# Optimization experiments

Hardware: AMD Instinct MI355X
Metric: run time of the kernel (lower is better)

## Reference

```python
import jax, jax.numpy as jnp
import numpy as np

N = 50000   # nodes
E = 800000  # edges (avg degree 16)
C = 64      # in_channels == out_channels


def _linear_params(key, fan_in, fan_out):
    kw, kb = jax.random.split(key)
    s = 1.0 / np.sqrt(fan_in)
    W = jax.random.uniform(kw, (fan_out, fan_in), minval=-s, maxval=s, dtype=jnp.float32)
    b = jax.random.uniform(kb, (fan_out,), minval=-s, maxval=s, dtype=jnp.float32)
    return W, b


def setup_inputs() -> dict:
    key = jax.random.key(0)
    ks = jax.random.split(key, 12)
    scalar = jax.random.normal(ks[0], (N, C), dtype=jnp.float32)
    vector = jax.random.normal(ks[1], (N, 3, C), dtype=jnp.float32)
    position = jax.random.normal(ks[2], (N, 3), dtype=jnp.float32)
    edge_index = jax.random.randint(ks[3], (2, E), 0, N, dtype=jnp.int64)
    edge_attr = jax.random.uniform(ks[4], (E,), dtype=jnp.float32)
    # Scalar_Conv params
    Wss, bss = _linear_params(ks[5], 2 * C, C)   # s_to_s
    Wvs, bvs = _linear_params(ks[6], 2 * C, C)   # v_to_s
    Wsl, bsl = _linear_params(ks[7], 2 * C, C)   # scalar_linear
    # Vector_Conv params
    Wsv, bsv = _linear_params(ks[8], 2 * C, C)   # s_to_v
    Wvv, bvv = _linear_params(ks[9], 2 * C, C)   # v_to_v
    Wvl, bvl = _linear_params(ks[10], 2 * C, C)  # vector_linear
    return dict(scalar=scalar, vector=vector, position=position,
                edge_index=edge_index, edge_attr=edge_attr,
                Wss=Wss, bss=bss, Wvs=Wvs, bvs=bvs, Wsl=Wsl, bsl=bsl,
                Wsv=Wsv, bsv=bsv, Wvv=Wvv, bvv=bvv, Wvl=Wvl, bvl=bvl)


def _norm(edge_index, edge_attr, num_nodes):
    # B=True path: edge_attr-weighted symmetric degree normalization
    row, col = edge_index[0], edge_index[1]
    deg = jax.ops.segment_sum(edge_attr, col, num_segments=num_nodes)
    deg_safe = jnp.where(deg > 0, deg, 1.0)
    dis = jnp.where(deg > 0, deg_safe ** -0.5, 0.0)
    return row, col, dis[row] * dis[col] * edge_attr


def _forward(scalar, vector, position, edge_index, edge_attr,
             Wss, bss, Wvs, bvs, Wsl, bsl, Wsv, bsv, Wvv, bvv, Wvl, bvl):
    num_nodes = scalar.shape[0]
    row, col = _norm(edge_index, edge_attr, num_nodes)[:2]
    _, _, norm = _norm(edge_index, edge_attr, num_nodes)
    # PyG: _i = target (col), _j = source (row); aggregate at col
    s_i, s_j = scalar[col], scalar[row]            # [E,C]
    v_i, v_j = vector[col], vector[row]            # [E,3,C]
    pos = position[col] - position[row]            # [E,3]
    s_cat = jnp.concatenate([s_i, s_j], axis=-1)   # [E,2C]
    v_cat = jnp.concatenate([v_i, v_j], axis=-1)   # [E,3,2C]

    # ---- Scalar_Conv messages ----
    s2s = jax.nn.silu(s_cat @ Wss.T + bss)                          # [E,C]
    v2s = v_cat @ Wvs.T + bvs                                       # [E,3,C]
    v2s = jax.nn.silu(jnp.sum(v2s * pos[:, :, None], axis=1))       # [E,C]
    s_msg = (jnp.concatenate([s2s, v2s], axis=-1) @ Wsl.T + bsl)    # [E,C]
    s_msg = norm[:, None] * s_msg
    s_agg = jax.ops.segment_sum(s_msg, col, num_segments=num_nodes)

    # ---- Vector_Conv messages ----
    s2v = s_cat @ Wsv.T + bsv                                       # [E,C]
    s2v = jnp.tanh(s2v[:, None, :] * pos[:, :, None])               # [E,3,C]
    v2v = v_cat @ Wvv.T + bvv                                       # [E,3,C]
    v_msg = jnp.concatenate([v2v, s2v], axis=-1) @ Wvl.T + bvl      # [E,3,C]
    v_msg = norm[:, None, None] * v_msg
    v_agg = jax.ops.segment_sum(v_msg, col, num_segments=num_nodes)

    scalar_out = jax.nn.silu(s_agg) + scalar
    vector_out = jnp.tanh(v_agg) + vector
    return scalar_out, vector_out


def reference(scalar, vector, position, edge_index, edge_attr,
              Wss, bss, Wvs, bvs, Wsl, bsl, Wsv, bsv, Wvv, bvv, Wvl, bvl):
    return _forward(scalar, vector, position, edge_index, edge_attr,
                    Wss, bss, Wvs, bvs, Wsl, bsl, Wsv, bsv, Wvv, bvv, Wvl, bvl)
```

## Files before the change

### kernel.cpp

```cpp
#include <hip/hip_runtime.h>
#include <cstdint>
#include <cstddef>

typedef unsigned int   u32;
typedef unsigned short u16;
typedef __attribute__((ext_vector_type(8))) short bf16x8;
typedef __attribute__((ext_vector_type(4))) float f32x4;

__device__ __forceinline__ float bf2f(u32 bits16) { return __uint_as_float(bits16 << 16); }
__device__ __forceinline__ u16 f2bf(float f) {
  u32 u = __float_as_uint(f);
  u = u + 0x7FFFu + ((u >> 16) & 1u);
  return (u16)(u >> 16);
}
__device__ __forceinline__ u32 pk(float a, float b) {
  return (u32)f2bf(a) | ((u32)f2bf(b) << 16);
}
__device__ __forceinline__ float lo16(u32 w) { return bf2f(w & 0xFFFFu); }
__device__ __forceinline__ float hi16(u32 w) { return bf2f(w >> 16); }
__device__ __forceinline__ float frcp(float x) { return __builtin_amdgcn_rcpf(x); }
__device__ __forceinline__ float fexp2(float x) { return __builtin_amdgcn_exp2f(x); }

#define NL2E   (-1.4426950408889634f)
#define TWOL2E (2.8853900817779268f)
#define CNTSC  1073741824.0

__device__ __forceinline__ int load_idx(const int* eidx, int is64, long long pos) {
  if (is64) return (int)(((const long long*)eidx)[pos]);
  return eidx[pos];
}

__global__ void k_prep1(const float* Wvl, const float* Wvv,
                        const float* bvv, const float* bvl,
                        const int* eidx, int E, int* flag,
                        float* WcTmp, float* bc,
                        double* dpk, int* erecI, int N) {
  int b = blockIdx.x, tid = threadIdx.x;
  if (b < 32) {
    int c = 2 * b + (tid >> 7), kk = tid & 127;
    float s = 0.f;
    for (int m = 0; m < 64; ++m) s += Wvl[c * 128 + m] * Wvv[m * 128 + kk];
    WcTmp[c * 128 + kk] = s;
  } else if (b == 32) {
    __shared__ int zc;
    if (tid == 0) zc = 0;
    __syncthreads();
    int n = (E < 1024) ? E : 1024;
    int local = 0;
    for (int i = tid; i < n; i += 256) {
      if (eidx[2 * i + 1] == 0) local++;
    }
    atomicAdd(&zc, local);
    __syncthreads();
    if (tid == 0) *flag = (zc >= (n >> 1)) ? 1 : 0;
  } else if (b == 33) {
    if (tid < 64) {
      float s = 0.f;
      for (int m = 0; m < 64; ++m) s += Wvl[tid * 128 + m] * bvv[m];
      bc[tid] = s + bvl[tid];
    }
  } else if (b == 34) {
    if (tid < 64) erecI[E + tid] = 0;
  } else {
    int idx = (b - 35) * 256 + tid;
    if (idx < N) dpk[idx] = 0.0;
  }
}

__global__ void k_prep2(const float* Wss, const float* Wsv, const float* Wvs,
                        const float* Wsl, const float* Wvl, const float* WcTmp,
                        u32* Wsl2, u32* Wpk, u16* Wtg) {
  int b = blockIdx.x, tid = threadIdx.x;
  if (b < 2) {
    for (int i = 0; i < 8; ++i) {
      int o = b * 2048 + i * 256 + tid;
      int h = o & 1, c = (o >> 1) & 63, g = o >> 7;
      int k = 4 * g + 2 * h;
      Wsl2[o] = pk(Wsl[c * 128 + k], Wsl[c * 128 + k + 1]);
    }
  } else if (b == 2) {
    for (int i = 0; i < 8; ++i) {
      int o = i * 256 + tid;
      int h = o & 1, c = (o >> 1) & 63, g = o >> 7;
      int k = 4 * g + 2 * h;
      Wpk[o] = pk(Wvl[c * 128 + 64 + k], Wvl[c * 128 + 64 + k + 1]);
    }
  } else {
    for (int i = 0; i < 16; ++i) {
      int p = (b - 3) * 4096 + i * 256 + tid;
      int r = p >> 6, k = p & 63;
      int g = (r >> 6) & 3, ch = r & 63;
      int src = ch * 128 + ((g & 2) ? 64 : 0) + k;
      float w;
      if (r < 256) w = (g & 1) ? Wsv[src] : Wss[src];
      else         w = (g & 1) ? WcTmp[src] : Wvs[src];
      u16 h = f2bf(w);
      Wtg[r * 128 + k] = h;
      Wtg[r * 128 + 64 + k] = f2bf(w - bf2f(h));
    }
  }
}

__global__ void k_scan_red(const double* dpk, int* blocksum, float* dis, int N) {
  __shared__ int lds[256];
  int tid = threadIdx.x, idx = blockIdx.x * 256 + tid;
  int c = 0;
  if (idx < N) {
    double p = dpk[idx];
    c = (int)(p * (1.0 / CNTSC));
    float dg = (float)(p - (double)c * CNTSC);
    dis[idx] = (dg > 0.f) ? rsqrtf(dg) : 0.f;
  }
  lds[tid] = c;
  __syncthreads();
  for (int off = 128; off > 0; off >>= 1) {
    if (tid < off) lds[tid] += lds[tid + off];
    __syncthreads();
  }
  if (tid == 0) blocksum[blockIdx.x] = lds[0];
}

__global__ void k_scan_mid(const int* blocksum, int* blockoff, int NB, int* rowptr, int N, int E) {
  __shared__ int lds[1024];
  int tid = threadIdx.x;
  int v = (tid < NB) ? blocksum[tid] : 0;
  lds[tid] = v;
  __syncthreads();
  for (int off = 1; off < 1024; off <<= 1) {
    int t = (tid >= off) ? lds[tid - off] : 0;
    __syncthreads();
    lds[tid] += t;
    __syncthreads();
  }
  if (tid < NB) blockoff[tid] = lds[tid] - v;
  if (tid == 0) rowptr[N] = E;
}

__global__ void k_scan_out(const double* dpk, const int* blockoff, int* rowptr, int* cursor, int N) {
  __shared__ int lds[256];
  int tid = threadIdx.x, idx = blockIdx.x * 256 + tid;
  int v = (idx < N) ? (int)(dpk[idx] * (1.0 / CNTSC)) : 0;
  lds[tid] = v;
  __syncthreads();
  for (int off = 1; off < 256; off <<= 1) {
    int t = (tid >= off) ? lds[tid - off] : 0;
    __syncthreads();
    lds[tid] += t;
    __syncthreads();
  }
  if (idx < N) {
    int o = blockoff[blockIdx.x] + lds[tid] - v;
    rowptr[idx] = o;
    cursor[idx] = o;
  }
}

__global__ void k_fill(const int* eidx, const int* flag, const float* attr, const float* dis,
                       const float* pos, int* cursor, float4* erecA, int* erecI, int E) {
  int e = blockIdx.x * 256 + threadIdx.x;
  if (e >= E) return;
  int is64 = *flag;
  int r  = load_idx(eidx, is64, e);
  int cl = load_idx(eidx, is64, (long long)E + e);
  float wr = dis[r] * attr[e];
  float dx = pos[cl * 3 + 0] - pos[r * 3 + 0];
  float dy = pos[cl * 3 + 1] - pos[r * 3 + 1];
  float dz = pos[cl * 3 + 2] - pos[r * 3 + 2];
  int p = atomicAdd(&cursor[cl], 1);
  erecA[p] = make_float4(wr, dx, dy, dz);
  erecI[p] = r;
}

__global__ __launch_bounds__(512, 4) void k_gemm_deg(
    const float* __restrict__ scalar, const float* __restrict__ vector,
    const u16* __restrict__ Wtg,
    uint4* __restrict__ rec_i4, uint4* __restrict__ rec_j4, int N, int GB,
    const int* __restrict__ eidx, const int* __restrict__ flag,
    const float* __restrict__ attr, double* __restrict__ dpk, int E) {
  __shared__ u32 smem[8192];
  int tid = threadIdx.x;
  if ((int)blockIdx.x >= GB) {
    int e = ((int)blockIdx.x - GB) * 512 + tid;
    if (e < E) {
      int is64 = *flag;
      int col = load_idx(eidx, is64, (long long)E + e);
      atomicAdd(&dpk[col], (double)attr[e] + CNTSC);
    }
    return;
  }
  u16*   Ax = (u16*)smem;
  float* Ep = (float*)smem;
  int lane = tid & 63, wv = tid >> 6;
  int nb = blockIdx.x * 32;

  {
    int srow = tid >> 2, skq = tid & 3;
    const float* sp;
    int snode;
    if (srow < 32) { snode = nb + srow; sp = scalar + (size_t)snode * 64 + skq * 16; }
    else {
      int d = (srow - 32) >> 5, nl2 = (srow - 32) & 31;
      snode = nb + nl2;
      sp = vector + (size_t)snode * 192 + d * 64 + skq * 16;
    }
    bool valid = snode < N;
    u16 hi[16], lo[16];
    #pragma unroll
    for (int q = 0; q < 4; ++q) {
      float4 v = valid ? *(const float4*)(sp + 4 * q) : make_float4(0.f, 0.f, 0.f, 0.f);
      float xs[4] = {v.x, v.y, v.z, v.w};
      #pragma unroll
      for (int j = 0; j < 4; ++j) {
        u16 h = f2bf(xs[j]);
        hi[4 * q + j] = h;
        lo[4 * q + j] = f2bf(xs[j] - bf2f(h));
      }
    }
    int rs = srow & 7;
    #pragma unroll
    for (int c = 0; c < 2; ++c) {
      int lc = 2 * skq + c;
      uint4 wh, wl;
      wh.x = (u32)hi[8*c+0] | ((u32)hi[8*c+1] << 16);
      wh.y = (u32)hi[8*c+2] | ((u32)hi[8*c+3] << 16);
      wh.z = (u32)hi[8*c+4] | ((u32)hi[8*c+5] << 16);
      wh.w = (u32)hi[8*c+6] | ((u32)hi[8*c+7] << 16);
      wl.x = (u32)lo[8*c+0] | ((u32)lo[8*c+1] << 16);
      wl.y = (u32)lo[8*c+2] | ((u32)lo[8*c+3] << 16);
      wl.z = (u32)lo[8*c+4] | ((u32)lo[8*c+5] << 16);
      wl.w = (u32)lo[8*c+6] | ((u32)lo[8*c+7] << 16);
      *(uint4*)(Ax + srow * 128 + (lc ^ rs) * 8)        = wh;
      *(uint4*)(Ax + srow * 128 + ((8 + lc) ^ rs) * 8)  = wl;
    }
  }
  __syncthreads();

  int c0 = wv * 32;
  int bl = lane & 15, bh = lane >> 4;
  f32x4 acc[8][2];
  #pragma unroll
  for (int mt = 0; mt < 8; ++mt)
    #pragma unroll
    for (int nt = 0; nt < 2; ++nt)
      acc[mt][nt] = (f32x4){0.f, 0.f, 0.f, 0.f};

  #pragma unroll
  for (int kh = 0; kh < 2; ++kh) {
    int k0 = kh * 32;
    bf16x8 Bh[2][2], Bl[2][2];
    #pragma unroll
    for (int rg = 0; rg < 2; ++rg)
      #pragma unroll
      for (int nt = 0; nt < 2; ++nt) {
        size_t rr = (size_t)(rg * 256 + c0 + nt * 16 + bl) * 128 + k0 + bh * 8;
        Bh[rg][nt] = *(const bf16x8*)(Wtg + rr);
        Bl[rg][nt] = *(const bf16x8*)(Wtg + rr + 64);
      }
    #pragma unroll
    for (int mt = 0; mt < 8; ++mt) {
      int row = mt * 16 + bl;
      int ch = (k0 >> 3) + bh, rs = row & 7;
      bf16x8 Ah = *(const bf16x8*)(Ax + row * 128 + (ch ^ rs) * 8);
      bf16x8 Al = *(const bf16x8*)(Ax + row * 128 + ((8 + ch) ^ rs) * 8);
      int rg = (mt < 2) ? 0 : 1;
      #pragma unroll
      for (int nt = 0; nt < 2; ++nt) {
        f32x4 a = acc[mt][nt];
        a = __builtin_amdgcn_mfma_f32_16x16x32_bf16(Ah, Bh[rg][nt], a, 0, 0, 0);
        a = __builtin_amdgcn_mfma_f32_16x16x32_bf16(Al, Bh[rg][nt], a, 0, 0, 0);
        a = __builtin_amdgcn_mfma_f32_16x16x32_bf16(Ah, Bl[rg][nt], a, 0, 0, 0);
        acc[mt][nt] = a;
      }
    }
  }

  int ech = tid & 63, eng = tid >> 6;
  uint4 oi[4], oj[4];
  #pragma unroll
  for (int pg = 0; pg < 4; ++pg) {
    __syncthreads();
    #pragma unroll
    for (int mm = 0; mm < 2; ++mm) {
      int mt = 2 * pg + mm;
      #pragma unroll
      for (int nt = 0; nt < 2; ++nt)
        #pragma unroll
        for (int r = 0; r < 4; ++r) {
          int rl = mm * 16 + bh * 4 + r;
          Ep[rl * 256 + c0 + nt * 16 + bl] = acc[mt][nt][r];
        }
    }
    __syncthreads();
    #pragma unroll
    for (int q = 0; q < 4; ++q) {
      int nl2 = eng + 8 * q;
      float vi0 = Ep[nl2 * 256 + ech];
      float vi1 = Ep[nl2 * 256 + 64 + ech];
      float vj0 = Ep[nl2 * 256 + 128 + ech];
      float vj1 = Ep[nl2 * 256 + 192 + ech];
      if (pg == 0) {
        oi[q].x = pk(vi0, vi1);                  oj[q].x = pk(vj0, vj1);
      } else if (pg == 1) {
        oi[q].y = (u32)f2bf(vi0);                oj[q].y = (u32)f2bf(vj0);
        oi[q].z = (u32)f2bf(vi1) << 16;          oj[q].z = (u32)f2bf(vj1) << 16;
      } else if (pg == 2) {
        oi[q].y |= (u32)f2bf(vi0) << 16;         oj[q].y |= (u32)f2bf(vj0) << 16;
        oi[q].w = (u32)f2bf(vi1);                oj[q].w = (u32)f2bf(vj1);
      } else {
        oi[q].z |= (u32)f2bf(vi0);               oj[q].z |= (u32)f2bf(vj0);
        oi[q].w |= (u32)f2bf(vi1) << 16;         oj[q].w |= (u32)f2bf(vj1) << 16;
      }
    }
  }
  #pragma unroll
  for (int q = 0; q < 4; ++q) {
    int node = nb + eng + 8 * q;
    if (node < N) {
      rec_i4[(size_t)node * 64 + ech] = oi[q];
      rec_j4[(size_t)node * 64 + ech] = oj[q];
    }
  }
}

__global__ __launch_bounds__(512) void k_edges(
    const u16* __restrict__ rec_i, const u16* __restrict__ rec_j,
    const float4* __restrict__ erecA, const int* __restrict__ erecI,
    const int* __restrict__ rowptr, const float* __restrict__ dis,
    const float* __restrict__ scalar, const float* __restrict__ vector,
    const float* __restrict__ bss, const float* __restrict__ bvs,
    const float* __restrict__ bsv, const float* __restrict__ bsl,
    const u32* __restrict__ Wsl2g, const u32* __restrict__ Wpkg,
    const float* __restrict__ bcg,
    float* __restrict__ out_s, float* __restrict__ out_v, int N) {
  __shared__ u32 sWsl[4096];
  __shared__ u32 sWv[2048];
  __shared__ float sStage[8 * 128];
  int tid = threadIdx.x, lane = tid & 63, wv = tid >> 6;
  for (int o = tid; o < 4096; o += 512) sWsl[o] = Wsl2g[o];
  for (int o = tid; o < 2048; o += 512) sWv[o] = Wpkg[o];
  __syncthreads();

  int node = __builtin_amdgcn_readfirstlane((int)(blockIdx.x * 8) + wv);
  if (node >= N) node = N - 1;

  uint4 riv = *(const uint4*)(rec_i + ((size_t)node << 9) + lane * 8);
  float aiB  = lo16(riv.x) + bss[lane];
  float KciB = TWOL2E * (hi16(riv.x) + bsv[lane]);
  float Bvs  = bvs[lane];
  float bib0 = lo16(riv.y) + Bvs;
  float bib1 = hi16(riv.y) + Bvs;
  float bib2 = lo16(riv.z) + Bvs;
  float Pi0  = hi16(riv.z), Pi1 = lo16(riv.w), Pi2 = hi16(riv.w);
  float bsl_c = bsl[lane], bc_c = bcg[lane];
  float disc = dis[node];

  float us = 0, uv = 0, t0 = 0, t1 = 0, t2 = 0, g0 = 0, g1 = 0, g2 = 0, wa = 0;
  int rp = rowptr[node], re = rowptr[node + 1];
  u32 lane16 = (u32)lane << 4;
  const char* rjb = (const char*)rec_j;

  u32 ra = (u32)erecI[rp];
  u32 rb = (u32)erecI[rp + 1];
  uint4 pre0 = *(const uint4*)(rjb + ((ra << 10) + lane16));
  uint4 pre1 = *(const uint4*)(rjb + ((rb << 10) + lane16));
  int p = rp;
  #define EDGE_MATH(CUR, EV)                                                  \
    {                                                                         \
      float nrm = EV.x, dx = EV.y, dy = EV.z, dz = EV.w;                      \
      float aj  = lo16(CUR.x), cj  = hi16(CUR.x);                             \
      float bj0 = lo16(CUR.y), bj1 = hi16(CUR.y), bj2 = lo16(CUR.z);          \
      float rj0 = hi16(CUR.z), rj1 = lo16(CUR.w), rj2 = hi16(CUR.w);          \
      float xs  = aiB + aj;                                                   \
      float s2s = xs * frcp(1.f + fexp2(xs * NL2E));                          \
      float yv  = (bib0 + bj0) * dx;                                          \
      yv = fmaf(bib1 + bj1, dy, yv);                                          \
      yv = fmaf(bib2 + bj2, dz, yv);                                          \
      float v2s = yv * frcp(1.f + fexp2(yv * NL2E));                          \
      float qh  = fmaf(TWOL2E, cj, KciB);                                     \
      float th0 = fmaf(-2.f, frcp(1.f + fexp2(qh * dx)), 1.f);                \
      float th1 = fmaf(-2.f, frcp(1.f + fexp2(qh * dy)), 1.f);                \
      float th2 = fmaf(-2.f, frcp(1.f + fexp2(qh * dz)), 1.f);                \
      us = fmaf(nrm, s2s, us); uv = fmaf(nrm, v2s, uv);                       \
      t0 = fmaf(nrm, th0, t0); t1 = fmaf(nrm, th1, t1); t2 = fmaf(nrm, th2, t2);\
      g0 = fmaf(nrm, rj0, g0); g1 = fmaf(nrm, rj1, g1); g2 = fmaf(nrm, rj2, g2);\
      wa += nrm;                                                              \
    }
  for (; p + 1 < re; p += 2) {
    uint4 cur0 = pre0, cur1 = pre1;
    u32 rn0 = (u32)erecI[p + 2];
    u32 rn1 = (u32)erecI[p + 3];
    pre0 = *(const uint4*)(rjb + ((rn0 << 10) + lane16));
    pre1 = *(const uint4*)(rjb + ((rn1 << 10) + lane16));
    float4 e0 = erecA[p];
    float4 e1 = erecA[p + 1];
    EDGE_MATH(cur0, e0)
    EDGE_MATH(cur1, e1)
  }
  if (p < re) {
    uint4 cur0 = pre0;
    float4 e0 = erecA[p];
    EDGE_MATH(cur0, e0)
  }
  #undef EDGE_MATH

  us *= disc; uv *= disc;
  t0 *= disc; t1 *= disc; t2 *= disc;
  g0 *= disc; g1 *= disc; g2 *= disc;
  wa *= disc;

  float* mys = &sStage[wv * 128];
  mys[lane] = us; mys[64 + lane] = uv;
  __threadfence_block();
  float acc = wa * bsl_c;
  #pragma unroll
  for (int g = 0; g < 32; ++g) {
    float4 u = *(const float4*)&mys[4 * g];
    uint2 w = *(const uint2*)&sWsl[(g * 64 + lane) * 2];
    acc = fmaf(u.x, lo16(w.x), acc);
    acc = fmaf(u.y, hi16(w.x), acc);
    acc = fmaf(u.z, lo16(w.y), acc);
    acc = fmaf(u.w, hi16(w.y), acc);
  }
  size_t so = ((size_t)node << 6) + lane;
  out_s[so] = acc * frcp(1.f + fexp2(acc * NL2E)) + scalar[so];

  float gg[3] = {g0, g1, g2}, tt[3] = {t0, t1, t2}, Pi[3] = {Pi0, Pi1, Pi2};
  #pragma unroll
  for (int d = 0; d < 3; ++d) {
    size_t vo = (((size_t)node * 3 + d) << 6) + lane;
    float vid = vector[vo];
    __threadfence_block();
    mys[lane] = tt[d];
    __threadfence_block();
    float a2 = fmaf(wa, bc_c + Pi[d], gg[d]);
    #pragma unroll
    for (int g = 0; g < 16; ++g) {
      float4 tu = *(const float4*)&mys[4 * g];
      uint2 w = *(const uint2*)&sWv[(g * 64 + lane) * 2];
      a2 = fmaf(tu.x, lo16(w.x), a2); a2 = fmaf(tu.y, hi16(w.x), a2);
      a2 = fmaf(tu.z, lo16(w.y), a2); a2 = fmaf(tu.w, hi16(w.y), a2);
    }
    float th = fmaf(-2.f, frcp(1.f + fexp2(TWOL2E * a2)), 1.f);
    out_v[vo] = th + vid;
  }
}

extern "C" void kernel_launch(void* const* d_in, const int* in_sizes, int n_in,
                              void* d_out, int out_size, void* d_ws, size_t ws_size,
                              hipStream_t stream) {
  const float* scalar   = (const float*)d_in[0];
  const float* vector   = (const float*)d_in[1];
  const float* position = (const float*)d_in[2];
  const int*   eidx     = (const int*)d_in[3];
  const float* attr     = (const float*)d_in[4];
  const float* Wss = (const float*)d_in[5];
  const float* bss = (const float*)d_in[6];
  const float* Wvs = (const float*)d_in[7];
  const float* bvs = (const float*)d_in[8];
  const float* Wsl = (const float*)d_in[9];
  const float* bsl = (const float*)d_in[10];
  const float* Wsv = (const float*)d_in[11];
  const float* bsv = (const float*)d_in[12];
  const float* Wvv = (const float*)d_in[13];
  const float* bvv = (const float*)d_in[14];
  const float* Wvl = (const float*)d_in[15];
  const float* bvl = (const float*)d_in[16];

  int N = in_sizes[0] / 64;
  int E = in_sizes[4];
  int NB = (N + 255) / 256;

  char* wsb = (char*)d_ws;
  size_t off = 0;
  auto alloc = [&](size_t bytes) -> char* {
    char* p = wsb + off;
    off += (bytes + 255) & ~(size_t)255;
    return p;
  };
  double* dpk    = (double*)alloc((size_t)N * 8);
  int*    rowptr = (int*)alloc((size_t)(N + 1) * 4);
  int*    cursor = (int*)alloc((size_t)N * 4);
  float*  dis    = (float*)alloc((size_t)N * 4);
  int*    blocksum = (int*)alloc((size_t)NB * 4);
  int*    blockoff = (int*)alloc((size_t)NB * 4);
  float4* erecA  = (float4*)alloc((size_t)E * 16);
  int*    erecI  = (int*)alloc((size_t)(E + 64) * 4);
  u16*    rec_i  = (u16*)alloc((size_t)N * 512 * 2);
  u16*    rec_j  = (u16*)alloc((size_t)N * 512 * 2);
  u16*    Wtg    = (u16*)alloc(512 * 128 * 2);
  u32*    Wsl2   = (u32*)alloc(4096 * 4);
  u32*    Wpk    = (u32*)alloc(2048 * 4);
  float*  WcTmp  = (float*)alloc(64 * 128 * 4);
  float*  bc     = (float*)alloc(64 * 4);
  int*    flag   = (int*)alloc(4);
  (void)ws_size; (void)n_in; (void)out_size;

  int GB = (N + 31) / 32;
  int DB = (E + 511) / 512;

  k_prep1<<<35 + NB, 256, 0, stream>>>(Wvl, Wvv, bvv, bvl, eidx, E, flag,
                                       WcTmp, bc, dpk, erecI, N);
  k_prep2<<<11, 256, 0, stream>>>(Wss, Wsv, Wvs, Wsl, Wvl, WcTmp, Wsl2, Wpk, Wtg);
  k_gemm_deg<<<GB + DB, 512, 0, stream>>>(scalar, vector, Wtg,
                                          (uint4*)rec_i, (uint4*)rec_j, N, GB,
                                          eidx, flag, attr, dpk, E);
  k_scan_red<<<NB, 256, 0, stream>>>(dpk, blocksum, dis, N);
  k_scan_mid<<<1, 1024, 0, stream>>>(blocksum, blockoff, NB, rowptr, N, E);
  k_scan_out<<<NB, 256, 0, stream>>>(dpk, blockoff, rowptr, cursor, N);
  k_fill<<<(E + 255) / 256, 256, 0, stream>>>(eidx, flag, attr, dis, position, cursor, erecA, erecI, E);
  k_edges<<<(N + 7) / 8, 512, 0, stream>>>(rec_i, rec_j, erecA, erecI, rowptr, dis,
                                           scalar, vector, bss, bvs, bsv, bsl,
                                           Wsl2, Wpk, bc,
                                           (float*)d_out, (float*)d_out + (size_t)N * 64, N);
}
```

Baseline: 405.4 us.

## Replace three-kernel scan with single-pass decoupled lookback; batch vector GEMV

The three scan kernels (block reduce, middle scan, output scan) are merged into one single-pass scan. Each block takes a tile id from an atomic counter and gets its exclusive prefix by chaining through per-tile status flags (decoupled lookback), which removes two launches and a pass over dpk. Separately, the three per-dimension vector GEMVs in k_edges now run in one loop that stages all three inputs in shared memory, so each weight load is reused three times and fewer block fences are needed. The lookback depends on earlier tiles making progress and adds serial spinning by thread 0, and the larger staging buffer raises shared memory use per block.

```diff
diff --git a/kernel.cpp b/kernel.cpp
--- a/kernel.cpp
+++ b/kernel.cpp
@@ -34,7 +34,8 @@
                         const float* bvv, const float* bvl,
                         const int* eidx, int E, int* flag,
                         float* WcTmp, float* bc,
-                        double* dpk, int* erecI, int N) {
+                        double* dpk, int* erecI, int* tilestat, int* tilectr,
+                        int N, int NB) {
   int b = blockIdx.x, tid = threadIdx.x;
   if (b < 32) {
     int c = 2 * b + (tid >> 7), kk = tid & 127;
@@ -61,6 +62,8 @@
     }
   } else if (b == 34) {
     if (tid < 64) erecI[E + tid] = 0;
+    if (tid == 64) *tilectr = 0;
+    for (int i = tid; i < NB; i += 256) tilestat[i] = 0;
   } else {
     int idx = (b - 35) * 256 + tid;
     if (idx < N) dpk[idx] = 0.0;
@@ -101,9 +104,15 @@
   }
 }
 
-__global__ void k_scan_red(const double* dpk, int* blocksum, float* dis, int N) {
+__global__ void k_scan(const double* dpk, float* dis, int* rowptr, int* cursor,
+                       int* tilestat, int* tilectr, int N, int E) {
   __shared__ int lds[256];
-  int tid = threadIdx.x, idx = blockIdx.x * 256 + tid;
+  __shared__ int sTile, sPrefix;
+  int tid = threadIdx.x;
+  if (tid == 0) sTile = atomicAdd(tilectr, 1);
+  __syncthreads();
+  int tile = sTile;
+  int idx = tile * 256 + tid;
   int c = 0;
   if (idx < N) {
     double p = dpk[idx];
@@ -113,43 +122,38 @@
   }
   lds[tid] = c;
   __syncthreads();
-  for (int off = 128; off > 0; off >>= 1) {
-    if (tid < off) lds[tid] += lds[tid + off];
-    __syncthreads();
-  }
-  if (tid == 0) blocksum[blockIdx.x] = lds[0];
-}
-
-__global__ void k_scan_mid(const int* blocksum, int* blockoff, int NB, int* rowptr, int N, int E) {
-  __shared__ int lds[1024];
-  int tid = threadIdx.x;
-  int v = (tid < NB) ? blocksum[tid] : 0;
-  lds[tid] = v;
-  __syncthreads();
-  for (int off = 1; off < 1024; off <<= 1) {
-    int t = (tid >= off) ? lds[tid - off] : 0;
-    __syncthreads();
-    lds[tid] += t;
-    __syncthreads();
-  }
-  if (tid < NB) blockoff[tid] = lds[tid] - v;
-  if (tid == 0) rowptr[N] = E;
-}
-
-__global__ void k_scan_out(const double* dpk, const int* blockoff, int* rowptr, int* cursor, int N) {
-  __shared__ int lds[256];
-  int tid = threadIdx.x, idx = blockIdx.x * 256 + tid;
-  int v = (idx < N) ? (int)(dpk[idx] * (1.0 / CNTSC)) : 0;
-  lds[tid] = v;
-  __syncthreads();
   for (int off = 1; off < 256; off <<= 1) {
     int t = (tid >= off) ? lds[tid - off] : 0;
     __syncthreads();
     lds[tid] += t;
     __syncthreads();
   }
+  int incl = lds[tid];
+  int aggregate = lds[255];
+  if (tid == 0) {
+    if (tile == 0) {
+      atomicExch(&tilestat[0], (2 << 30) | aggregate);
+      rowptr[N] = E;
+    } else {
+      atomicExch(&tilestat[tile], (1 << 30) | aggregate);
+      int excl = 0;
+      int t = tile - 1;
+      while (true) {
+        int s = atomicAdd(&tilestat[t], 0);
+        int flag = (u32)s >> 30;
+        if (flag == 0) continue;
+        excl += s & 0x3FFFFFFF;
+        if (flag == 2) break;
+        --t;
+      }
+      sPrefix = excl;
+      atomicExch(&tilestat[tile], (2 << 30) | (excl + aggregate));
+    }
+  }
+  __syncthreads();
+  int exclPrefix = (tile == 0) ? 0 : sPrefix;
   if (idx < N) {
-    int o = blockoff[blockIdx.x] + lds[tid] - v;
+    int o = exclPrefix + incl - c;
     rowptr[idx] = o;
     cursor[idx] = o;
   }
@@ -334,7 +338,7 @@
     float* __restrict__ out_s, float* __restrict__ out_v, int N) {
   __shared__ u32 sWsl[4096];
   __shared__ u32 sWv[2048];
-  __shared__ float sStage[8 * 128];
+  __shared__ float sStage[8 * 192];
   int tid = threadIdx.x, lane = tid & 63, wv = tid >> 6;
   for (int o = tid; o < 4096; o += 512) sWsl[o] = Wsl2g[o];
   for (int o = tid; o < 2048; o += 512) sWv[o] = Wpkg[o];
@@ -408,7 +412,7 @@
   g0 *= disc; g1 *= disc; g2 *= disc;
   wa *= disc;
 
-  float* mys = &sStage[wv * 128];
+  float* mys = &sStage[wv * 192];
   mys[lane] = us; mys[64 + lane] = uv;
   __threadfence_block();
   float acc = wa * bsl_c;
@@ -424,24 +428,32 @@
   size_t so = ((size_t)node << 6) + lane;
   out_s[so] = acc * frcp(1.f + fexp2(acc * NL2E)) + scalar[so];
 
-  float gg[3] = {g0, g1, g2}, tt[3] = {t0, t1, t2}, Pi[3] = {Pi0, Pi1, Pi2};
+  __threadfence_block();
+  mys[lane] = t0; mys[64 + lane] = t1; mys[128 + lane] = t2;
+  __threadfence_block();
+  float a20 = fmaf(wa, bc_c + Pi0, g0);
+  float a21 = fmaf(wa, bc_c + Pi1, g1);
+  float a22 = fmaf(wa, bc_c + Pi2, g2);
+  #pragma unroll
+  for (int g = 0; g < 16; ++g) {
+    float4 u0 = *(const float4*)&mys[4 * g];
+    float4 u1 = *(const float4*)&mys[64 + 4 * g];
+    float4 u2 = *(const float4*)&mys[128 + 4 * g];
+    uint2 w = *(const uint2*)&sWv[(g * 64 + lane) * 2];
+    float w0 = lo16(w.x), w1 = hi16(w.x), w2 = lo16(w.y), w3 = hi16(w.y);
+    a20 = fmaf(u0.x, w0, a20); a20 = fmaf(u0.y, w1, a20);
+    a20 = fmaf(u0.z, w2, a20); a20 = fmaf(u0.w, w3, a20);
+    a21 = fmaf(u1.x, w0, a21); a21 = fmaf(u1.y, w1, a21);
+    a21 = fmaf(u1.z, w2, a21); a21 = fmaf(u1.w, w3, a21);
+    a22 = fmaf(u2.x, w0, a22); a22 = fmaf(u2.y, w1, a22);
+    a22 = fmaf(u2.z, w2, a22); a22 = fmaf(u2.w, w3, a22);
+  }
+  float a2v[3] = {a20, a21, a22};
   #pragma unroll
   for (int d = 0; d < 3; ++d) {
     size_t vo = (((size_t)node * 3 + d) << 6) + lane;
-    float vid = vector[vo];
-    __threadfence_block();
-    mys[lane] = tt[d];
-    __threadfence_block();
-    float a2 = fmaf(wa, bc_c + Pi[d], gg[d]);
-    #pragma unroll
-    for (int g = 0; g < 16; ++g) {
-      float4 tu = *(const float4*)&mys[4 * g];
-      uint2 w = *(const uint2*)&sWv[(g * 64 + lane) * 2];
-      a2 = fmaf(tu.x, lo16(w.x), a2); a2 = fmaf(tu.y, hi16(w.x), a2);
-      a2 = fmaf(tu.z, lo16(w.y), a2); a2 = fmaf(tu.w, hi16(w.y), a2);
-    }
-    float th = fmaf(-2.f, frcp(1.f + fexp2(TWOL2E * a2)), 1.f);
-    out_v[vo] = th + vid;
+    float th = fmaf(-2.f, frcp(1.f + fexp2(TWOL2E * a2v[d])), 1.f);
+    out_v[vo] = th + vector[vo];
   }
 }
 
@@ -481,8 +493,8 @@
   int*    rowptr = (int*)alloc((size_t)(N + 1) * 4);
   int*    cursor = (int*)alloc((size_t)N * 4);
   float*  dis    = (float*)alloc((size_t)N * 4);
-  int*    blocksum = (int*)alloc((size_t)NB * 4);
-  int*    blockoff = (int*)alloc((size_t)NB * 4);
+  int*    tilestat = (int*)alloc((size_t)NB * 4);
+  int*    tilectr  = (int*)alloc(4);
   float4* erecA  = (float4*)alloc((size_t)E * 16);
   int*    erecI  = (int*)alloc((size_t)(E + 64) * 4);
   u16*    rec_i  = (u16*)alloc((size_t)N * 512 * 2);
@@ -499,14 +511,12 @@
   int DB = (E + 511) / 512;
 
   k_prep1<<<35 + NB, 256, 0, stream>>>(Wvl, Wvv, bvv, bvl, eidx, E, flag,
-                                       WcTmp, bc, dpk, erecI, N);
+                                       WcTmp, bc, dpk, erecI, tilestat, tilectr, N, NB);
   k_prep2<<<11, 256, 0, stream>>>(Wss, Wsv, Wvs, Wsl, Wvl, WcTmp, Wsl2, Wpk, Wtg);
   k_gemm_deg<<<GB + DB, 512, 0, stream>>>(scalar, vector, Wtg,
                                           (uint4*)rec_i, (uint4*)rec_j, N, GB,
                                           eidx, flag, attr, dpk, E);
-  k_scan_red<<<NB, 256, 0, stream>>>(dpk, blocksum, dis, N);
-  k_scan_mid<<<1, 1024, 0, stream>>>(blocksum, blockoff, NB, rowptr, N, E);
-  k_scan_out<<<NB, 256, 0, stream>>>(dpk, blockoff, rowptr, cursor, N);
+  k_scan<<<NB, 256, 0, stream>>>(dpk, dis, rowptr, cursor, tilestat, tilectr, N, E);
   k_fill<<<(E + 255) / 256, 256, 0, stream>>>(eidx, flag, attr, dis, position, cursor, erecA, erecI, E);
   k_edges<<<(N + 7) / 8, 512, 0, stream>>>(rec_i, rec_j, erecA, erecI, rowptr, dis,
                                            scalar, vector, bss, bvs, bsv, bsl,
```

Result: no change. 404.5 us (-0.2%).
